# Kernel tuning notes

Measured on AMD Instinct MI355X. Metric: run time of the kernel, lower is better.

The kernel has to match this reference:

```python
import jax, jax.numpy as jnp
import numpy as np

IN_DIM = 256
OUT_DIM = 256
EMBED_DIM = 256
GROUPS = 8
BN_EPS = 1e-5


def conv2d(x, w, b, pad, groups=1):
    # x: NCHW, w: OIHW (I = in_ch / groups)
    out = jax.lax.conv_general_dilated(
        x, w, window_strides=(1, 1), padding=[(pad, pad), (pad, pad)],
        dimension_numbers=('NCHW', 'OIHW', 'NCHW'), feature_group_count=groups)
    return out + b[None, :, None, None]


def setup_inputs() -> dict:
    key = jax.random.key(0)
    ks = jax.random.split(key, 8)
    s = 0.05
    d = {}
    d['x'] = jax.random.normal(ks[0], (2, IN_DIM, 16, 16), jnp.float32)
    d['y'] = jax.random.normal(ks[1], (2, OUT_DIM, 128, 128), jnp.float32)
    # channle_reduce: Conv2d(256, 64, k=3, groups=64) -> weight (64, 4, 3, 3)
    d['w_cr'] = jax.random.normal(ks[2], (IN_DIM // 4, 4, 3, 3), jnp.float32) * s
    d['b_cr'] = jnp.zeros((IN_DIM // 4,), jnp.float32)
    # depthwise convs on 64 channels
    d['w_dw3'] = jax.random.normal(ks[3], (IN_DIM // 4, 1, 3, 3), jnp.float32) * s
    d['b_dw3'] = jnp.zeros((IN_DIM // 4,), jnp.float32)
    d['w_dw7'] = jax.random.normal(ks[4], (IN_DIM // 4, 1, 5, 5), jnp.float32) * s
    d['b_dw7'] = jnp.zeros((IN_DIM // 4,), jnp.float32)
    # gate: Conv2d(256, 128, 1) + BN + StarReLU
    d['w_gate'] = jax.random.normal(ks[5], (IN_DIM // 2, IN_DIM, 1, 1), jnp.float32) * s
    d['b_gate'] = jnp.zeros((IN_DIM // 2,), jnp.float32)
    d['bn_gamma'] = jnp.ones((IN_DIM // 2,), jnp.float32)
    d['bn_beta'] = jnp.zeros((IN_DIM // 2,), jnp.float32)
    d['bn_mean'] = jnp.zeros((IN_DIM // 2,), jnp.float32)
    d['bn_var'] = jnp.ones((IN_DIM // 2,), jnp.float32)
    d['sr_scale'] = jnp.ones((1,), jnp.float32)
    d['sr_bias'] = jnp.zeros((1,), jnp.float32)
    # linear1: Linear(16, 8192) -> torch weight shape (8192, 16)
    d['w_lin'] = jax.random.normal(ks[6], (OUT_DIM * EMBED_DIM // GROUPS, IN_DIM // (2 * GROUPS)), jnp.float32) * s
    d['b_lin'] = jnp.zeros((OUT_DIM * EMBED_DIM // GROUPS,), jnp.float32)
    return d


def reference(x, y, w_cr, b_cr, w_dw3, b_dw3, w_dw7, b_dw7, w_gate, b_gate,
              bn_gamma, bn_beta, bn_mean, bn_var, sr_scale, sr_bias, w_lin, b_lin):
    B, C, H, Wd = x.shape
    # gate branch: 1x1 conv -> BN (inference stats) -> StarReLU
    g = conv2d(x, w_gate, b_gate, 0)
    inv = (bn_gamma / jnp.sqrt(bn_var + BN_EPS))[None, :, None, None]
    g = (g - bn_mean[None, :, None, None]) * inv + bn_beta[None, :, None, None]
    g = sr_scale * jnp.square(jnp.maximum(g, 0.0)) + sr_bias
    # feature branch
    xr = conv2d(x, w_cr, b_cr, 1, groups=IN_DIM // 4)        # (B, 64, H, W)
    x3 = conv2d(xr, w_dw3, b_dw3, 1, groups=IN_DIM // 4)
    x7 = conv2d(xr, w_dw7, b_dw7, 2, groups=IN_DIM // 4)
    xc = jnp.concatenate([x3, x7], axis=1) * g               # (B, 128, H, W)
    # per-pixel weight generation: (B,H,W,G,16) @ (16,8192)
    xc = xc.reshape(B, GROUPS, -1, H, Wd).transpose(0, 3, 4, 1, 2)
    wdec = jnp.einsum('bhwgi,oi->bhwgo', xc, w_lin) + b_lin  # (B,H,W,8,8192)
    # flatten (G, out*embed/G) -> (embed, out); matches torch reshape order
    wdec = wdec.reshape(B, H, Wd, EMBED_DIM, OUT_DIM)
    # patch-wise dynamic 1x1 conv == per-patch batched matmul
    b, c, h, w = y.shape
    fh, fw = H, Wd
    ph, pw = h // fh, w // fw
    yp = y.reshape(b, c, fh, ph, fw, pw)
    # out[b,e,f,p,g,q] = sum_c wdec[b,f,g,e,c] * y[b,c,f,p,g,q]
    out = jnp.einsum('bfgec,bcfpgq->befpgq', wdec, yp)
    return out.reshape(b, EMBED_DIM, h, w)
```

## Files before the change

### kernel.cpp

```cpp
#include <hip/hip_runtime.h>
#include <stdint.h>


typedef __attribute__((ext_vector_type(8))) short short8;
typedef __attribute__((ext_vector_type(4))) float f32x4;

#define BN_EPS 1e-5f

__device__ __forceinline__ unsigned short f2bf(float f) {
  unsigned u = __float_as_uint(f);
  return (unsigned short)((u + 0x8000u) >> 16);
}
__device__ __forceinline__ unsigned pk2bf(float a, float b) {
  unsigned ua = __float_as_uint(a), ub = __float_as_uint(b);
  return ((ua + 0x8000u) >> 16) | ((ub + 0x8000u) & 0xFFFF0000u);
}

__global__ __launch_bounds__(256) void k1a_groupconv(
    const float* __restrict__ x, const float* __restrict__ w_cr,
    const float* __restrict__ b_cr, float* __restrict__ xr)
{
  __shared__ float xs[4][256];
  int b = blockIdx.x >> 6, cr = blockIdx.x & 63;
  int t = threadIdx.x;
  {
    int ch = t >> 6, off = (t & 63) * 4;
    float4 v = *(const float4*)(x + b * 65536 + (cr * 4 + ch) * 256 + off);
    *(float4*)&xs[ch][off] = v;
  }
  __syncthreads();
  int h = t >> 4, w = t & 15;
  float a = b_cr[cr];
  #pragma unroll
  for (int ii = 0; ii < 4; ++ii) {
    const float* wp = w_cr + (cr * 4 + ii) * 9;
    #pragma unroll
    for (int ky = 0; ky < 3; ++ky) {
      int gy = h + ky - 1;
      #pragma unroll
      for (int kx = 0; kx < 3; ++kx) {
        int gx = w + kx - 1;
        float v = (gy >= 0 && gy < 16 && gx >= 0 && gx < 16) ? xs[ii][gy * 16 + gx] : 0.f;
        a += wp[ky * 3 + kx] * v;
      }
    }
  }
  xr[(b * 64 + cr) * 256 + t] = a;
}

__global__ __launch_bounds__(256) void k1b_gate_dw(
    const float* __restrict__ x, const float* __restrict__ xr,
    const float* __restrict__ w_dw3, const float* __restrict__ b_dw3,
    const float* __restrict__ w_dw7, const float* __restrict__ b_dw7,
    const float* __restrict__ w_gate, const float* __restrict__ b_gate,
    const float* __restrict__ bn_gamma, const float* __restrict__ bn_beta,
    const float* __restrict__ bn_mean, const float* __restrict__ bn_var,
    const float* __restrict__ sr_scale, const float* __restrict__ sr_bias,
    const float* __restrict__ w_lin, short* __restrict__ wlin_bf, short* __restrict__ xc_bf)
{
  __shared__ float xcen[256];
  __shared__ float gs[128];
  int blk = blockIdx.x;
  int b = blk >> 8, h = (blk >> 4) & 15, w = blk & 15;
  int t = threadIdx.x;

  { int idx = blk * 256 + t; wlin_bf[idx] = (short)f2bf(w_lin[idx]); }

  xcen[t] = x[b * 65536 + t * 256 + h * 16 + w];
  __syncthreads();

  int o = t >> 1, half = t & 1;
  {
    const float* wrow = w_gate + o * 256 + half * 128;
    const float* xcn  = xcen + half * 128;
    float ga = 0.f;
    #pragma unroll 8
    for (int ci = 0; ci < 128; ci += 4) {
      float4 wv = *(const float4*)(wrow + ci);
      float4 xv = *(const float4*)(xcn + ci);
      ga += wv.x * xv.x + wv.y * xv.y + wv.z * xv.z + wv.w * xv.w;
    }
    ga += __shfl_xor(ga, 1);
    float inv = bn_gamma[o] * rsqrtf(bn_var[o] + BN_EPS);
    float gg = (ga + b_gate[o] - bn_mean[o]) * inv + bn_beta[o];
    gg = fmaxf(gg, 0.f);
    gg = sr_scale[0] * gg * gg + sr_bias[0];
    if (half == 0) gs[o] = gg;
  }
  __syncthreads();

  if (t < 128) {
    int oc = t;
    float f0;
    if (oc < 64) {
      f0 = b_dw3[oc];
      const float* wp = w_dw3 + oc * 9;
      const float* xp = xr + (b * 64 + oc) * 256;
      #pragma unroll
      for (int ky = 0; ky < 3; ++ky) {
        int gy = h + ky - 1;
        #pragma unroll
        for (int kx = 0; kx < 3; ++kx) {
          int gx = w + kx - 1;
          float v = (gy >= 0 && gy < 16 && gx >= 0 && gx < 16) ? xp[gy * 16 + gx] : 0.f;
          f0 += wp[ky * 3 + kx] * v;
        }
      }
    } else {
      int c5 = oc - 64;
      f0 = b_dw7[c5];
      const float* wp = w_dw7 + c5 * 25;
      const float* xp = xr + (b * 64 + c5) * 256;
      #pragma unroll
      for (int ky = 0; ky < 5; ++ky) {
        int gy = h + ky - 2;
        #pragma unroll
        for (int kx = 0; kx < 5; ++kx) {
          int gx = w + kx - 2;
          float v = (gy >= 0 && gy < 16 && gx >= 0 && gx < 16) ? xp[gy * 16 + gx] : 0.f;
          f0 += wp[ky * 5 + kx] * v;
        }
      }
    }
    int pix = (b * 16 + h) * 16 + w;
    xc_bf[pix * 128 + oc] = (short)f2bf(f0 * gs[oc]);
  }
}

__global__ __launch_bounds__(512, 4) void k2_fused(
    const float* __restrict__ y, const short* __restrict__ wlin_bf,
    const short* __restrict__ xc_bf, const float* __restrict__ b_lin,
    float* __restrict__ out)
{
  __shared__ __align__(16) short Ylds[16384];
  __shared__ __align__(16) float scratch[8192];
  short* wdlds = (short*)scratch;

  int phys = blockIdx.x;
  int blk = (phys & 7) * 64 + (phys >> 3);
  int b = blk >> 8, f = (blk >> 4) & 15, g = blk & 15;
  int tid = threadIdx.x;
  int wave = tid >> 6, lane = tid & 63;
  int quad = lane >> 4, l16 = lane & 15;

  const float* yb = y + b * 4194304 + (f * 8) * 128 + g * 8;

  int c32 = tid >> 4, pf = tid & 15;
  for (int sch = 0; sch < 2; ++sch) {
    float4 v[4];
    #pragma unroll
    for (int it = 0; it < 4; ++it)
      v[it] = *(const float4*)(yb + (sch * 128 + it * 32 + c32) * 16384 + (pf >> 1) * 128 + (pf & 1) * 4);
    #pragma unroll
    for (int it = 0; it < 4; ++it)
      *(float4*)&scratch[(it * 32 + c32) * 64 + pf * 4] = v[it];
    __syncthreads();
    #pragma unroll
    for (int tt = 0; tt < 2; ++tt) {
      int task = tt * 512 + tid;
      int pix = task & 63, cg = task >> 6;
      float s0 = scratch[(cg * 8 + 0) * 64 + pix];
      float s1 = scratch[(cg * 8 + 1) * 64 + pix];
      float s2 = scratch[(cg * 8 + 2) * 64 + pix];
      float s3 = scratch[(cg * 8 + 3) * 64 + pix];
      float s4 = scratch[(cg * 8 + 4) * 64 + pix];
      float s5 = scratch[(cg * 8 + 5) * 64 + pix];
      float s6 = scratch[(cg * 8 + 6) * 64 + pix];
      float s7 = scratch[(cg * 8 + 7) * 64 + pix];
      uint4 pk;
      pk.x = pk2bf(s0, s1); pk.y = pk2bf(s2, s3);
      pk.z = pk2bf(s4, s5); pk.w = pk2bf(s6, s7);
      int chunk = sch * 16 + cg;
      int physc = chunk ^ (pix & 7);
      *(uint4*)&Ylds[pix * 256 + physc * 8] = pk;
    }
    __syncthreads();
  }

  short8 bx = {0, 0, 0, 0, 0, 0, 0, 0};
  if (quad < 2 && l16 < 8)
    bx = *(const short8*)(xc_bf + blk * 128 + l16 * 16 + quad * 8);

  f32x4 zero4 = {0.f, 0.f, 0.f, 0.f};
  f32x4 acc[2][4];
  #pragma unroll
  for (int et = 0; et < 2; ++et)
    #pragma unroll
    for (int nt = 0; nt < 4; ++nt)
      acc[et][nt] = zero4;

  auto gen_chunk = [&](int cc, int buf) {
    short* dst = wdlds + buf * 8192;
    #pragma unroll
    for (int jj = 0; jj < 4; ++jj) {
      int j = wave * 4 + jj;
      #pragma unroll
      for (int hh = 0; hh < 2; ++hh) {
        int c0 = cc * 32 + hh * 16;
        short8 aw = {0, 0, 0, 0, 0, 0, 0, 0};
        if (quad < 2)
          aw = *(const short8*)(wlin_bf + (j * 256 + c0 + l16) * 16 + quad * 8);
        f32x4 d = __builtin_amdgcn_mfma_f32_16x16x32_bf16(aw, bx, zero4, 0, 0, 0);
        if (l16 < 8) {
          int e = l16 * 32 + j;
          float4 bl = *(const float4*)(b_lin + j * 256 + c0 + quad * 4);
          uint2 pk;
          pk.x = pk2bf(d[0] + bl.x, d[1] + bl.y);
          pk.y = pk2bf(d[2] + bl.z, d[3] + bl.w);
          int q16 = hh * 2 + (quad >> 1);
          int sw = q16 ^ ((e >> 1) & 3) ^ ((e >> 5) & 3);
          *(uint2*)&dst[e * 32 + sw * 8 + (quad & 1) * 4] = pk;
        }
      }
    }
  };

  gen_chunk(0, 0);
  __syncthreads();

  for (int cc = 0; cc < 8; ++cc) {
    if (cc < 7) gen_chunk(cc + 1, (cc + 1) & 1);

    const short* src = wdlds + (cc & 1) * 8192;
    short8 A2[2], Bf[4];
    #pragma unroll
    for (int et = 0; et < 2; ++et) {
      int e = wave * 32 + et * 16 + l16;
      int sw = quad ^ ((e >> 1) & 3) ^ ((e >> 5) & 3);
      A2[et] = *(const short8*)&src[e * 32 + sw * 8];
    }
    int chunkY = cc * 4 + quad;
    #pragma unroll
    for (int nt = 0; nt < 4; ++nt) {
      int nn = nt * 16 + l16;
      int physc = chunkY ^ (nn & 7);
      Bf[nt] = *(const short8*)&Ylds[nn * 256 + physc * 8];
    }
    #pragma unroll
    for (int et = 0; et < 2; ++et)
      #pragma unroll
      for (int nt = 0; nt < 4; ++nt)
        acc[et][nt] = __builtin_amdgcn_mfma_f32_16x16x32_bf16(A2[et], Bf[nt], acc[et][nt], 0, 0, 0);
    __syncthreads();
  }

  float* ob = out + b * 4194304 + (f * 8) * 128 + g * 8;
  #pragma unroll
  for (int et = 0; et < 2; ++et) {
    int e0 = wave * 32 + et * 16 + quad * 4;
    #pragma unroll
    for (int nt = 0; nt < 4; ++nt) {
      int pix = nt * 16 + l16;
      float* oa = ob + (pix >> 3) * 128 + (pix & 7);
      #pragma unroll
      for (int r = 0; r < 4; ++r)
        oa[(e0 + r) * 16384] = acc[et][nt][r];
    }
  }
}

extern "C" void kernel_launch(void* const* d_in, const int* in_sizes, int n_in,
                              void* d_out, int out_size, void* d_ws, size_t ws_size,
                              hipStream_t stream) {
  const float* x        = (const float*)d_in[0];
  const float* y        = (const float*)d_in[1];
  const float* w_cr     = (const float*)d_in[2];
  const float* b_cr     = (const float*)d_in[3];
  const float* w_dw3    = (const float*)d_in[4];
  const float* b_dw3    = (const float*)d_in[5];
  const float* w_dw7    = (const float*)d_in[6];
  const float* b_dw7    = (const float*)d_in[7];
  const float* w_gate   = (const float*)d_in[8];
  const float* b_gate   = (const float*)d_in[9];
  const float* bn_gamma = (const float*)d_in[10];
  const float* bn_beta  = (const float*)d_in[11];
  const float* bn_mean  = (const float*)d_in[12];
  const float* bn_var   = (const float*)d_in[13];
  const float* sr_scale = (const float*)d_in[14];
  const float* sr_bias  = (const float*)d_in[15];
  const float* w_lin    = (const float*)d_in[16];
  const float* b_lin    = (const float*)d_in[17];
  float* out = (float*)d_out;

  short* xc_bf   = (short*)d_ws;
  short* wlin_bf = (short*)((char*)d_ws + 131072);
  float* xr      = (float*)((char*)d_ws + 131072 + 262144);

  hipLaunchKernelGGL(k1a_groupconv, dim3(128), dim3(256), 0, stream, x, w_cr, b_cr, xr);
  hipLaunchKernelGGL(k1b_gate_dw, dim3(512), dim3(256), 0, stream,
                     x, xr, w_dw3, b_dw3, w_dw7, b_dw7, w_gate, b_gate,
                     bn_gamma, bn_beta, bn_mean, bn_var, sr_scale, sr_bias,
                     w_lin, wlin_bf, xc_bf);
  hipLaunchKernelGGL(k2_fused, dim3(512), dim3(512), 0, stream,
                     y, wlin_bf, xc_bf, b_lin, out);
}
```

Before: 168.4 us.

## Merge front-end kernels and split main kernel over embed halves

```diff
diff --git a/kernel.cpp b/kernel.cpp
--- a/kernel.cpp
+++ b/kernel.cpp
@@ -16,129 +16,136 @@
   return ((ua + 0x8000u) >> 16) | ((ub + 0x8000u) & 0xFFFF0000u);
 }
 
-__global__ __launch_bounds__(256) void k1a_groupconv(
+__global__ __launch_bounds__(256) void k1_merged(
     const float* __restrict__ x, const float* __restrict__ w_cr,
-    const float* __restrict__ b_cr, float* __restrict__ xr)
+    const float* __restrict__ b_cr, const float* __restrict__ w_dw3,
+    const float* __restrict__ b_dw3, const float* __restrict__ w_dw7,
+    const float* __restrict__ b_dw7, const float* __restrict__ w_gate,
+    const float* __restrict__ b_gate, const float* __restrict__ bn_gamma,
+    const float* __restrict__ bn_beta, const float* __restrict__ bn_mean,
+    const float* __restrict__ bn_var, const float* __restrict__ sr_scale,
+    const float* __restrict__ sr_bias, const float* __restrict__ w_lin,
+    short* __restrict__ wlin_bf, float* __restrict__ f0_out,
+    float* __restrict__ gs_out)
 {
-  __shared__ float xs[4][256];
-  int b = blockIdx.x >> 6, cr = blockIdx.x & 63;
+  __shared__ __align__(16) float xcen[256];
+  __shared__ __align__(16) float xs[4][256];
+  __shared__ __align__(16) float xrs[256];
+
+  int blk = blockIdx.x;
   int t = threadIdx.x;
-  {
-    int ch = t >> 6, off = (t & 63) * 4;
-    float4 v = *(const float4*)(x + b * 65536 + (cr * 4 + ch) * 256 + off);
-    *(float4*)&xs[ch][off] = v;
-  }
-  __syncthreads();
-  int h = t >> 4, w = t & 15;
-  float a = b_cr[cr];
-  #pragma unroll
-  for (int ii = 0; ii < 4; ++ii) {
-    const float* wp = w_cr + (cr * 4 + ii) * 9;
-    #pragma unroll
-    for (int ky = 0; ky < 3; ++ky) {
-      int gy = h + ky - 1;
-      #pragma unroll
-      for (int kx = 0; kx < 3; ++kx) {
-        int gx = w + kx - 1;
-        float v = (gy >= 0 && gy < 16 && gx >= 0 && gx < 16) ? xs[ii][gy * 16 + gx] : 0.f;
-        a += wp[ky * 3 + kx] * v;
-      }
-    }
-  }
-  xr[(b * 64 + cr) * 256 + t] = a;
-}
-
-__global__ __launch_bounds__(256) void k1b_gate_dw(
-    const float* __restrict__ x, const float* __restrict__ xr,
-    const float* __restrict__ w_dw3, const float* __restrict__ b_dw3,
-    const float* __restrict__ w_dw7, const float* __restrict__ b_dw7,
-    const float* __restrict__ w_gate, const float* __restrict__ b_gate,
-    const float* __restrict__ bn_gamma, const float* __restrict__ bn_beta,
-    const float* __restrict__ bn_mean, const float* __restrict__ bn_var,
-    const float* __restrict__ sr_scale, const float* __restrict__ sr_bias,
-    const float* __restrict__ w_lin, short* __restrict__ wlin_bf, short* __restrict__ xc_bf)
-{
-  __shared__ float xcen[256];
-  __shared__ float gs[128];
-  int blk = blockIdx.x;
-  int b = blk >> 8, h = (blk >> 4) & 15, w = blk & 15;
-  int t = threadIdx.x;
-
-  { int idx = blk * 256 + t; wlin_bf[idx] = (short)f2bf(w_lin[idx]); }
-
-  xcen[t] = x[b * 65536 + t * 256 + h * 16 + w];
-  __syncthreads();
-
-  int o = t >> 1, half = t & 1;
-  {
-    const float* wrow = w_gate + o * 256 + half * 128;
-    const float* xcn  = xcen + half * 128;
-    float ga = 0.f;
-    #pragma unroll 8
-    for (int ci = 0; ci < 128; ci += 4) {
-      float4 wv = *(const float4*)(wrow + ci);
-      float4 xv = *(const float4*)(xcn + ci);
-      ga += wv.x * xv.x + wv.y * xv.y + wv.z * xv.z + wv.w * xv.w;
-    }
-    ga += __shfl_xor(ga, 1);
-    float inv = bn_gamma[o] * rsqrtf(bn_var[o] + BN_EPS);
-    float gg = (ga + b_gate[o] - bn_mean[o]) * inv + bn_beta[o];
-    gg = fmaxf(gg, 0.f);
-    gg = sr_scale[0] * gg * gg + sr_bias[0];
-    if (half == 0) gs[o] = gg;
-  }
-  __syncthreads();
-
-  if (t < 128) {
-    int oc = t;
-    float f0;
-    if (oc < 64) {
-      f0 = b_dw3[oc];
-      const float* wp = w_dw3 + oc * 9;
-      const float* xp = xr + (b * 64 + oc) * 256;
+
+  if (blk < 512) {
+    int b = blk >> 8, h = (blk >> 4) & 15, w = blk & 15;
+    int pix = (b * 16 + h) * 16 + w;
+
+    { int idx = blk * 256 + t; wlin_bf[idx] = (short)f2bf(w_lin[idx]); }
+
+    xcen[t] = x[b * 65536 + t * 256 + h * 16 + w];
+    __syncthreads();
+
+    int wave = t >> 6, lane = t & 63;
+    int oq = lane >> 2, ol = lane & 3;
+    const float4* wg4 = (const float4*)w_gate;
+    const float4* xc4 = (const float4*)xcen;
+    float ss = sr_scale[0], sb = sr_bias[0];
+
+    #pragma unroll
+    for (int pass = 0; pass < 2; ++pass) {
+      int o = wave * 32 + pass * 16 + oq;
+      float acc = 0.f;
+      #pragma unroll
+      for (int k = 0; k < 16; ++k) {
+        int j = k * 4 + ol;
+        float4 wv = wg4[o * 64 + j];
+        float4 xv = xc4[j];
+        acc += wv.x * xv.x + wv.y * xv.y + wv.z * xv.z + wv.w * xv.w;
+      }
+      acc += __shfl_xor(acc, 1);
+      acc += __shfl_xor(acc, 2);
+      float inv = bn_gamma[o] * rsqrtf(bn_var[o] + BN_EPS);
+      float gg = (acc + b_gate[o] - bn_mean[o]) * inv + bn_beta[o];
+      gg = fmaxf(gg, 0.f);
+      gg = ss * gg * gg + sb;
+      if (ol == 0) gs_out[pix * 128 + o] = gg;
+    }
+  } else {
+    int cb = blk - 512;
+    int b = cb >> 6, cr = cb & 63;
+    {
+      int ch = t >> 6, off = (t & 63) * 4;
+      float4 v = *(const float4*)(x + b * 65536 + (cr * 4 + ch) * 256 + off);
+      *(float4*)&xs[ch][off] = v;
+    }
+    __syncthreads();
+    int h = t >> 4, w = t & 15;
+    float a = b_cr[cr];
+    #pragma unroll
+    for (int ii = 0; ii < 4; ++ii) {
+      const float* wp = w_cr + (cr * 4 + ii) * 9;
       #pragma unroll
       for (int ky = 0; ky < 3; ++ky) {
         int gy = h + ky - 1;
         #pragma unroll
         for (int kx = 0; kx < 3; ++kx) {
           int gx = w + kx - 1;
-          float v = (gy >= 0 && gy < 16 && gx >= 0 && gx < 16) ? xp[gy * 16 + gx] : 0.f;
-          f0 += wp[ky * 3 + kx] * v;
+          float v = (gy >= 0 && gy < 16 && gx >= 0 && gx < 16) ? xs[ii][gy * 16 + gx] : 0.f;
+          a += wp[ky * 3 + kx] * v;
         }
       }
-    } else {
-      int c5 = oc - 64;
-      f0 = b_dw7[c5];
-      const float* wp = w_dw7 + c5 * 25;
-      const float* xp = xr + (b * 64 + c5) * 256;
+    }
+    xrs[t] = a;
+    __syncthreads();
+
+    float f3 = b_dw3[cr];
+    {
+      const float* wp = w_dw3 + cr * 9;
+      #pragma unroll
+      for (int ky = 0; ky < 3; ++ky) {
+        int gy = h + ky - 1;
+        #pragma unroll
+        for (int kx = 0; kx < 3; ++kx) {
+          int gx = w + kx - 1;
+          float v = (gy >= 0 && gy < 16 && gx >= 0 && gx < 16) ? xrs[gy * 16 + gx] : 0.f;
+          f3 += wp[ky * 3 + kx] * v;
+        }
+      }
+    }
+    float f5 = b_dw7[cr];
+    {
+      const float* wp = w_dw7 + cr * 25;
       #pragma unroll
       for (int ky = 0; ky < 5; ++ky) {
         int gy = h + ky - 2;
         #pragma unroll
         for (int kx = 0; kx < 5; ++kx) {
           int gx = w + kx - 2;
-          float v = (gy >= 0 && gy < 16 && gx >= 0 && gx < 16) ? xp[gy * 16 + gx] : 0.f;
-          f0 += wp[ky * 5 + kx] * v;
+          float v = (gy >= 0 && gy < 16 && gx >= 0 && gx < 16) ? xrs[gy * 16 + gx] : 0.f;
+          f5 += wp[ky * 5 + kx] * v;
         }
       }
     }
     int pix = (b * 16 + h) * 16 + w;
-    xc_bf[pix * 128 + oc] = (short)f2bf(f0 * gs[oc]);
-  }
-}
-
-__global__ __launch_bounds__(512, 4) void k2_fused(
+    f0_out[pix * 128 + cr] = f3;
+    f0_out[pix * 128 + 64 + cr] = f5;
+  }
+}
+
+__global__ __launch_bounds__(512, 6) void k2_fused(
     const float* __restrict__ y, const short* __restrict__ wlin_bf,
-    const short* __restrict__ xc_bf, const float* __restrict__ b_lin,
-    float* __restrict__ out)
+    const float* __restrict__ f0_in, const float* __restrict__ gs_in,
+    const float* __restrict__ b_lin, float* __restrict__ out)
 {
   __shared__ __align__(16) short Ylds[16384];
-  __shared__ __align__(16) float scratch[8192];
-  short* wdlds = (short*)scratch;
+  __shared__ __align__(16) char dyn[16384];
+  float* scratch = (float*)dyn;
+  short* wdbuf = (short*)dyn;
 
   int phys = blockIdx.x;
-  int blk = (phys & 7) * 64 + (phys >> 3);
-  int b = blk >> 8, f = (blk >> 4) & 15, g = blk & 15;
+  int logical = (phys & 7) * 128 + (phys >> 3);
+  int patch = logical >> 1, ehalf = logical & 1;
+  int b = patch >> 8, f = (patch >> 4) & 15, g = patch & 15;
+  int gbase = ehalf * 4;
   int tid = threadIdx.x;
   int wave = tid >> 6, lane = tid & 63;
   int quad = lane >> 4, l16 = lane & 15;
@@ -146,19 +153,17 @@
   const float* yb = y + b * 4194304 + (f * 8) * 128 + g * 8;
 
   int c32 = tid >> 4, pf = tid & 15;
-  for (int sch = 0; sch < 2; ++sch) {
-    float4 v[4];
-    #pragma unroll
-    for (int it = 0; it < 4; ++it)
-      v[it] = *(const float4*)(yb + (sch * 128 + it * 32 + c32) * 16384 + (pf >> 1) * 128 + (pf & 1) * 4);
-    #pragma unroll
-    for (int it = 0; it < 4; ++it)
+  for (int sch = 0; sch < 4; ++sch) {
+    float4 v[2];
+    #pragma unroll
+    for (int it = 0; it < 2; ++it)
+      v[it] = *(const float4*)(yb + (sch * 64 + it * 32 + c32) * 16384 + (pf >> 1) * 128 + (pf & 1) * 4);
+    #pragma unroll
+    for (int it = 0; it < 2; ++it)
       *(float4*)&scratch[(it * 32 + c32) * 64 + pf * 4] = v[it];
     __syncthreads();
-    #pragma unroll
-    for (int tt = 0; tt < 2; ++tt) {
-      int task = tt * 512 + tid;
-      int pix = task & 63, cg = task >> 6;
+    {
+      int pix = tid & 63, cg = tid >> 6;
       float s0 = scratch[(cg * 8 + 0) * 64 + pix];
       float s1 = scratch[(cg * 8 + 1) * 64 + pix];
       float s2 = scratch[(cg * 8 + 2) * 64 + pix];
@@ -170,40 +175,48 @@
       uint4 pk;
       pk.x = pk2bf(s0, s1); pk.y = pk2bf(s2, s3);
       pk.z = pk2bf(s4, s5); pk.w = pk2bf(s6, s7);
-      int chunk = sch * 16 + cg;
+      int chunk = sch * 8 + cg;
       int physc = chunk ^ (pix & 7);
       *(uint4*)&Ylds[pix * 256 + physc * 8] = pk;
     }
     __syncthreads();
   }
 
+  int geff = l16 & 7, jsel = l16 >> 3;
+  bool bvalid = (geff < 4) && (jsel == (quad >> 1));
   short8 bx = {0, 0, 0, 0, 0, 0, 0, 0};
-  if (quad < 2 && l16 < 8)
-    bx = *(const short8*)(xc_bf + blk * 128 + l16 * 16 + quad * 8);
+  if (bvalid) {
+    const float* fp = f0_in + patch * 128 + (gbase + geff) * 16 + (quad & 1) * 8;
+    const float* gp = gs_in + patch * 128 + (gbase + geff) * 16 + (quad & 1) * 8;
+    float4 fa = *(const float4*)fp, fb = *(const float4*)(fp + 4);
+    float4 ga = *(const float4*)gp, gb = *(const float4*)(gp + 4);
+    bx[0] = (short)f2bf(fa.x * ga.x); bx[1] = (short)f2bf(fa.y * ga.y);
+    bx[2] = (short)f2bf(fa.z * ga.z); bx[3] = (short)f2bf(fa.w * ga.w);
+    bx[4] = (short)f2bf(fb.x * gb.x); bx[5] = (short)f2bf(fb.y * gb.y);
+    bx[6] = (short)f2bf(fb.z * gb.z); bx[7] = (short)f2bf(fb.w * gb.w);
+  }
 
   f32x4 zero4 = {0.f, 0.f, 0.f, 0.f};
-  f32x4 acc[2][4];
+  f32x4 acc[4];
   #pragma unroll
-  for (int et = 0; et < 2; ++et)
-    #pragma unroll
-    for (int nt = 0; nt < 4; ++nt)
-      acc[et][nt] = zero4;
-
+  for (int nt = 0; nt < 4; ++nt) acc[nt] = zero4;
+
+  int jA_half = quad >> 1;
   auto gen_chunk = [&](int cc, int buf) {
-    short* dst = wdlds + buf * 8192;
-    #pragma unroll
-    for (int jj = 0; jj < 4; ++jj) {
-      int j = wave * 4 + jj;
+    short* dst = wdbuf + buf * 4096;
+    #pragma unroll
+    for (int jj = 0; jj < 2; ++jj) {
+      int jp = wave * 2 + jj;
+      int jA = jp * 2 + jA_half;
+      int jD = jp * 2 + jsel;
       #pragma unroll
       for (int hh = 0; hh < 2; ++hh) {
         int c0 = cc * 32 + hh * 16;
-        short8 aw = {0, 0, 0, 0, 0, 0, 0, 0};
-        if (quad < 2)
-          aw = *(const short8*)(wlin_bf + (j * 256 + c0 + l16) * 16 + quad * 8);
+        short8 aw = *(const short8*)(wlin_bf + (jA * 256 + c0 + l16) * 16 + (quad & 1) * 8);
         f32x4 d = __builtin_amdgcn_mfma_f32_16x16x32_bf16(aw, bx, zero4, 0, 0, 0);
-        if (l16 < 8) {
-          int e = l16 * 32 + j;
-          float4 bl = *(const float4*)(b_lin + j * 256 + c0 + quad * 4);
+        if (geff < 4) {
+          int e = geff * 32 + jD;
+          float4 bl = *(const float4*)(b_lin + jD * 256 + c0 + quad * 4);
           uint2 pk;
           pk.x = pk2bf(d[0] + bl.x, d[1] + bl.y);
           pk.y = pk2bf(d[2] + bl.z, d[3] + bl.w);
@@ -221,13 +234,12 @@
   for (int cc = 0; cc < 8; ++cc) {
     if (cc < 7) gen_chunk(cc + 1, (cc + 1) & 1);
 
-    const short* src = wdlds + (cc & 1) * 8192;
-    short8 A2[2], Bf[4];
-    #pragma unroll
-    for (int et = 0; et < 2; ++et) {
-      int e = wave * 32 + et * 16 + l16;
+    const short* src = wdbuf + (cc & 1) * 4096;
+    short8 A2, Bf[4];
+    {
+      int e = wave * 16 + l16;
       int sw = quad ^ ((e >> 1) & 3) ^ ((e >> 5) & 3);
-      A2[et] = *(const short8*)&src[e * 32 + sw * 8];
+      A2 = *(const short8*)&src[e * 32 + sw * 8];
     }
     int chunkY = cc * 4 + quad;
     #pragma unroll
@@ -237,25 +249,20 @@
       Bf[nt] = *(const short8*)&Ylds[nn * 256 + physc * 8];
     }
     #pragma unroll
-    for (int et = 0; et < 2; ++et)
-      #pragma unroll
-      for (int nt = 0; nt < 4; ++nt)
-        acc[et][nt] = __builtin_amdgcn_mfma_f32_16x16x32_bf16(A2[et], Bf[nt], acc[et][nt], 0, 0, 0);
+    for (int nt = 0; nt < 4; ++nt)
+      acc[nt] = __builtin_amdgcn_mfma_f32_16x16x32_bf16(A2, Bf[nt], acc[nt], 0, 0, 0);
     __syncthreads();
   }
 
   float* ob = out + b * 4194304 + (f * 8) * 128 + g * 8;
+  int e0 = ehalf * 128 + wave * 16 + quad * 4;
   #pragma unroll
-  for (int et = 0; et < 2; ++et) {
-    int e0 = wave * 32 + et * 16 + quad * 4;
-    #pragma unroll
-    for (int nt = 0; nt < 4; ++nt) {
-      int pix = nt * 16 + l16;
-      float* oa = ob + (pix >> 3) * 128 + (pix & 7);
-      #pragma unroll
-      for (int r = 0; r < 4; ++r)
-        oa[(e0 + r) * 16384] = acc[et][nt][r];
-    }
+  for (int nt = 0; nt < 4; ++nt) {
+    int pix = nt * 16 + l16;
+    float* oa = ob + (pix >> 3) * 128 + (pix & 7);
+    #pragma unroll
+    for (int r = 0; r < 4; ++r)
+      oa[(e0 + r) * 16384] = acc[nt][r];
   }
 }
 
@@ -282,15 +289,14 @@
   const float* b_lin    = (const float*)d_in[17];
   float* out = (float*)d_out;
 
-  short* xc_bf   = (short*)d_ws;
-  short* wlin_bf = (short*)((char*)d_ws + 131072);
-  float* xr      = (float*)((char*)d_ws + 131072 + 262144);
-
-  hipLaunchKernelGGL(k1a_groupconv, dim3(128), dim3(256), 0, stream, x, w_cr, b_cr, xr);
-  hipLaunchKernelGGL(k1b_gate_dw, dim3(512), dim3(256), 0, stream,
-                     x, xr, w_dw3, b_dw3, w_dw7, b_dw7, w_gate, b_gate,
+  float* f0      = (float*)d_ws;
+  float* gs      = (float*)((char*)d_ws + 262144);
+  short* wlin_bf = (short*)((char*)d_ws + 524288);
+
+  hipLaunchKernelGGL(k1_merged, dim3(640), dim3(256), 0, stream,
+                     x, w_cr, b_cr, w_dw3, b_dw3, w_dw7, b_dw7, w_gate, b_gate,
                      bn_gamma, bn_beta, bn_mean, bn_var, sr_scale, sr_bias,
-                     w_lin, wlin_bf, xc_bf);
-  hipLaunchKernelGGL(k2_fused, dim3(512), dim3(512), 0, stream,
-                     y, wlin_bf, xc_bf, b_lin, out);
-}
+                     w_lin, wlin_bf, f0, gs);
+  hipLaunchKernelGGL(k2_fused, dim3(1024), dim3(512), 0, stream,
+                     y, wlin_bf, f0, gs, b_lin, out);
+}
```

Result: no change. 167.6 us (-0.5%).
